# Kernel optimization log

Measured on AMD Instinct MI355X. Metric: run time of the kernel, lower is better.

The kernel has to match this reference:

```python
import jax, jax.numpy as jnp
import numpy as np

EMBED_DIM = 1024
HEADS = 16
HEAD_DIM = EMBED_DIM // HEADS
BATCH = 4
SEQ = 1024


def setup_inputs() -> dict:
    key = jax.random.key(0)
    ks = jax.random.split(key, 9)
    s = 1.0 / np.sqrt(HEAD_DIM)
    so = 1.0 / np.sqrt(EMBED_DIM)
    return {
        "values": jax.random.normal(ks[0], (BATCH, SEQ, EMBED_DIM), dtype=jnp.float32),
        "query": jax.random.normal(ks[1], (BATCH, SEQ, EMBED_DIM), dtype=jnp.float32),
        "key": jax.random.normal(ks[2], (BATCH, SEQ, EMBED_DIM), dtype=jnp.float32),
        "mask": jax.random.randint(ks[3], (BATCH, 1, SEQ, SEQ), 0, 2, dtype=jnp.int32),
        "Wv": jax.random.uniform(ks[4], (HEAD_DIM, HEAD_DIM), jnp.float32, -s, s),
        "Wk": jax.random.uniform(ks[5], (HEAD_DIM, HEAD_DIM), jnp.float32, -s, s),
        "Wq": jax.random.uniform(ks[6], (HEAD_DIM, HEAD_DIM), jnp.float32, -s, s),
        "Wo": jax.random.uniform(ks[7], (EMBED_DIM, EMBED_DIM), jnp.float32, -so, so),
        "bo": jax.random.uniform(ks[8], (EMBED_DIM,), jnp.float32, -so, so),
    }


def reference(values, query, key, mask, Wv, Wk, Wq, Wo, bo):
    N, Lq, E = query.shape
    Lk = key.shape[1]
    H, D = HEADS, HEAD_DIM
    # reshape to heads, then per-head shared linear projection (Linear(head_dim, head_dim), no bias)
    v = jnp.einsum('nlhd,ed->nlhe', values.reshape(N, Lk, H, D), Wv)
    k = jnp.einsum('nlhd,ed->nlhe', key.reshape(N, Lk, H, D), Wk)
    q = jnp.einsum('nlhd,ed->nlhe', query.reshape(N, Lq, H, D), Wq)
    # full [N,H,Q,K] scores, scaled by 1/sqrt(embed_dim) as in source
    sim = jnp.einsum('nqhd,nkhd->nhqk', q, k)
    sim = jnp.where(mask == 0, jnp.float32(-1e20), sim)
    attn = jax.nn.softmax(sim / jnp.sqrt(jnp.float32(E)), axis=3)
    out = jnp.einsum('nhqk,nkhd->nqhd', attn, v).reshape(N, Lq, H * D)
    return out @ Wo.T + bo
```

## Files before the change

kernel.cpp:

```cpp
#include <hip/hip_runtime.h>

#define SEQ 1024
#define HEADS 16
#define HD 64
#define EMB 1024

typedef short bf16x8 __attribute__((ext_vector_type(8)));
typedef float f32x4 __attribute__((ext_vector_type(4)));

static __device__ __forceinline__ unsigned cvtpk(float a, float b) {
  unsigned r;
  asm("v_cvt_pk_bf16_f32 %0, %1, %2" : "=v"(r) : "v"(a), "v"(b));
  return r;
}

static __device__ __forceinline__ void gload_lds16(const void* g, void* l) {
  __builtin_amdgcn_global_load_lds((const __attribute__((address_space(1))) unsigned int*)g,
                                   (__attribute__((address_space(3))) unsigned int*)l,
                                   16, 0, 0);
}

__global__ __launch_bounds__(256) void k_pp(const int* __restrict__ mask,
                                            const float* __restrict__ Wo,
                                            const float* __restrict__ Wv,
                                            const float* __restrict__ Wq,
                                            const float* __restrict__ Wk,
                                            const float* __restrict__ values,
                                            const float* __restrict__ query,
                                            const float* __restrict__ key,
                                            unsigned long long* __restrict__ mb,
                                            unsigned short* __restrict__ wob,
                                            unsigned short* __restrict__ vb,
                                            unsigned short* __restrict__ qb,
                                            unsigned short* __restrict__ kb) {
  __shared__ unsigned short Wl[64][64];
  const unsigned tid = threadIdx.x;
  const unsigned b = blockIdx.x;

  if (b < 3072) {
    const int lane = tid & 63, c = lane & 15, g = lane >> 4;
    const int wid = b * 4 + (tid >> 6);
    const int t = wid >> 12;
    const int rem = wid & 4095;
    const int n = rem >> 10, h = (rem >> 6) & 15, lb = rem & 63;

    const float* x; unsigned short* out;
// ... 62 lines not shown
    } else {
      unsigned short* op = out + ((size_t)(n * HEADS + h) * SEQ + lb * 16) * HD;
      #pragma unroll
      for (int r = 0; r < 4; ++r) {
        const unsigned w0 = cvtpk(acc[0][r], acc[1][r]);
        const unsigned w1 = cvtpk(acc[2][r], acc[3][r]);
        *(uint2*)(op + (4 * g + r) * HD + 4 * c) = make_uint2(w0, w1);
      }
    }
  } else if (b < 7168) {
    const unsigned lane = tid & 63u;
    const unsigned gwb = (b - 3072) * 16u + (tid >> 6) * 4u;
    #pragma unroll
    for (int it = 0; it < 4; ++it) {
      const unsigned gw = gwb + it;
      const int v = mask[(size_t)gw * 64u + lane];
      const unsigned long long bits = __ballot(v != 0);
      if (lane == 0) {
        const unsigned n = gw >> 14, qrow = (gw >> 4) & 1023u, ktile = gw & 15u;
        mb[((size_t)n * 16 + ktile) * 1024 + qrow] = bits;
      }
    }
  } else {
    const unsigned gid = (b - 7168) * 256u + tid;
    const unsigned e = gid >> 8, rem = gid & 255u;
    const unsigned blk = rem >> 4, cc = rem & 15u;
    const float* src = Wo + (size_t)e * 1024 + blk * 64 + cc;
    const unsigned w0 = cvtpk(src[0], src[16]);
    const unsigned w1 = cvtpk(src[32], src[48]);
    *(uint2*)(wob + (size_t)gid * 4) = make_uint2(w0, w1);
  }
}

__global__ __launch_bounds__(256, 2) void k_attn(const unsigned short* __restrict__ qb,
                                                 const unsigned short* __restrict__ kb,
                                                 const unsigned short* __restrict__ vb,
                                                 const unsigned long long* __restrict__ mb,
                                                 unsigned short* __restrict__ ob) {
  const int tid = threadIdx.x;
  const int w = tid >> 6, lane = tid & 63;
  const int c = lane & 15, g = lane >> 4;
  const int bid = blockIdx.x;
  const int nh = bid & 63, q128 = bid >> 6;
  const int n = nh >> 4, h = nh & 15;
  const int qlo = q128 * 128 + w * 32;

  __shared__ unsigned short Ks[2][2][64][64];
  __shared__ unsigned short Vs[2][2][64][64];

  char* const Kb0 = (char*)&Ks[0][0][0][0];
  char* const Vb0 = (char*)&Vs[0][0][0][0];

  const size_t nhb = (size_t)(n * HEADS + h) * (SEQ * HD);
  const unsigned short* qp = qb + nhb;
  const char* kpB = (const char*)(kb + nhb);
  const char* vpB = (const char*)(vb + nhb);

  const char* kSrc[4]; const char* vSrc[4]; int ldsOff[4];
  #pragma unroll
  for (int i = 0; i < 4; ++i) {
    const int off = i * 4096 + tid * 16;
    const int row = off >> 7;
    const int tile = row >> 6, r64 = row & 63;
    const int slot = (off >> 4) & 7;
    const int krow = ((r64 >> 4) & 1) * 32 + ((r64 >> 5) & 1) * 4 +
                     ((r64 >> 2) & 3) * 8 + (r64 & 3);
    const int sw = (slot ^ (r64 & 7)) << 4;
    kSrc[i] = kpB + (size_t)(tile * 64 + krow) * 128 + sw;
    vSrc[i] = vpB + (size_t)r64 * 2048 + tile * 128 + sw;
    ldsOff[i] = off;
  }

  bf16x8 qa[2][2];
  #pragma unroll
  for (int grp = 0; grp < 2; ++grp)
    #pragma unroll
    for (int ks = 0; ks < 2; ++ks)
      qa[grp][ks] = *(const bf16x8*)(qp + (size_t)(qlo + grp * 16 + c) * HD + ks * 32 + g * 8);

  bf16x8 ones;
  #pragma unroll
  for (int j = 0; j < 8; ++j) ones[j] = (short)0x3F80;

  f32x4 o[2][4] = {};
  f32x4 lacc[2] = {};

#define STAGEKV(dstK, dstV, kp_) do {                                    \
    _Pragma("unroll")                                                    \
    for (int i = 0; i < 4; ++i) {                                        \
      gload_lds16(kSrc[i] + (size_t)(kp_) * 16384, (dstK) + ldsOff[i]);  \
      gload_lds16(vSrc[i] + (kp_) * 256, (dstV) + ldsOff[i]);            \
    }                                                                    \
  } while (0)

  STAGEKV(Kb0, Vb0, 0);

  for (int kp = 0; kp < 8; ++kp) {
    const int cur = kp & 1;
    if (kp < 7) {
      STAGEKV(Kb0 + (cur ^ 1) * 16384, Vb0 + (cur ^ 1) * 16384, kp + 1);
      asm volatile("s_waitcnt vmcnt(8)" ::: "memory");
    } else {
      asm volatile("s_waitcnt vmcnt(0)" ::: "memory");
    }
    asm volatile("s_barrier" ::: "memory");

    #pragma unroll
    for (int t = 0; t < 2; ++t) {
      const int kt = kp * 2 + t;
      char* const Kc = Kb0 + cur * 16384 + t * 8192;
      char* const Vc = Vb0 + cur * 16384 + t * 8192;

      const unsigned long long bits0 = mb[((size_t)(n * 16 + kt)) * 1024 + qlo + c];
      const unsigned long long bits1 = mb[((size_t)(n * 16 + kt)) * 1024 + qlo + 16 + c];

      bf16x8 kf[4][2];
      #pragma unroll
      for (int sub = 0; sub < 4; ++sub) {
        const int rho = sub * 16 + c;
        #pragma unroll
        for (int ks = 0; ks < 2; ++ks)
          kf[sub][ks] = *(const bf16x8*)(Kc + rho * 128 + (((ks * 4 + g) ^ (c & 7)) << 4));
      }
      bf16x8 vf[4][2];
      #pragma unroll
      for (int db = 0; db < 4; ++db) {
        const int row = db * 16 + c;
        #pragma unroll
        for (int ks = 0; ks < 2; ++ks)
          vf[db][ks] = *(const bf16x8*)(Vc + row * 128 + (((ks * 4 + g) ^ (c & 7)) << 4));
      }

      #pragma unroll
      for (int grp = 0; grp < 2; ++grp) {
        const unsigned long long bits = grp ? bits1 : bits0;
        const unsigned blo = (unsigned)bits, bhi = (unsigned)(bits >> 32);

        f32x4 s[4];
        __builtin_amdgcn_s_setprio(1);
        #pragma unroll
        for (int sub = 0; sub < 4; ++sub) {
          f32x4 acc = {};
          acc = __builtin_amdgcn_mfma_f32_16x16x32_bf16(kf[sub][0], qa[grp][0], acc, 0, 0, 0);
          acc = __builtin_amdgcn_mfma_f32_16x16x32_bf16(kf[sub][1], qa[grp][1], acc, 0, 0, 0);
          s[sub] = acc;
        }
        __builtin_amdgcn_s_setprio(0);

        unsigned pw[2][4];
        #pragma unroll
        for (int sub = 0; sub < 4; ++sub) {
          const unsigned x = ((sub & 1) ? bhi : blo) >> (8 * g + ((sub >> 1) << 2));
          const float p0 = (x & 1u) ? __builtin_exp2f(s[sub][0]) : 0.f;
          const float p1 = (x & 2u) ? __builtin_exp2f(s[sub][1]) : 0.f;
          const float p2 = (x & 4u) ? __builtin_exp2f(s[sub][2]) : 0.f;
          const float p3 = (x & 8u) ? __builtin_exp2f(s[sub][3]) : 0.f;
          pw[sub & 1][(sub >> 1) * 2 + 0] = cvtpk(p0, p1);
          pw[sub & 1][(sub >> 1) * 2 + 1] = cvtpk(p2, p3);
        }
        bf16x8 pa[2];
        pa[0] = __builtin_bit_cast(bf16x8, *(uint4*)&pw[0][0]);
        pa[1] = __builtin_bit_cast(bf16x8, *(uint4*)&pw[1][0]);

        __builtin_amdgcn_s_setprio(1);
        #pragma unroll
        for (int ks = 0; ks < 2; ++ks) {
          #pragma unroll
          for (int db = 0; db < 4; ++db)
            o[grp][db] = __builtin_amdgcn_mfma_f32_16x16x32_bf16(pa[ks], vf[db][ks], o[grp][db], 0, 0, 0);
          lacc[grp] = __builtin_amdgcn_mfma_f32_16x16x32_bf16(pa[ks], ones, lacc[grp], 0, 0, 0);
        }
        __builtin_amdgcn_s_setprio(0);
      }
    }

    if (kp < 7) asm volatile("s_barrier" ::: "memory");
  }
#undef STAGEKV

  #pragma unroll
  for (int grp = 0; grp < 2; ++grp)
    #pragma unroll
    for (int r = 0; r < 4; ++r) {
      const float inv = 1.0f / lacc[grp][r];
      const unsigned w0 = cvtpk(o[grp][0][r] * inv, o[grp][1][r] * inv);
      const unsigned w1 = cvtpk(o[grp][2][r] * inv, o[grp][3][r] * inv);
      *(uint2*)(ob + ((size_t)n * SEQ + qlo + grp * 16 + 4 * g + r) * EMB + h * 64 + 4 * c) =
          make_uint2(w0, w1);
    }
}

__global__ __launch_bounds__(256, 2) void k_gemm(const unsigned short* __restrict__ A,
                                                 const unsigned short* __restrict__ B,
                                                 const float* __restrict__ bo,
                                                 float* __restrict__ C) {
  const int tid = threadIdx.x;
  const int w = tid >> 6, lane = tid & 63;
  const int c = lane & 15, g = lane >> 4;
  const int bm = blockIdx.x & 31, bn = blockIdx.x >> 5;
  const int m0 = bm * 128, n0 = bn * 64;

  __shared__ unsigned short As[2][128][64];
  __shared__ unsigned short Bs[2][64][64];

  const char* aSrc[4]; int aOff[4];
  const char* bSrc[2]; int bOff[2];
  #pragma unroll
  for (int i = 0; i < 4; ++i) {
    const int off = i * 4096 + tid * 16;
    const int row = off >> 7, slot = (off >> 4) & 7;
    const int sw = (slot ^ (row & 7)) << 4;
    aSrc[i] = (const char*)A + (size_t)(m0 + row) * 2048 + sw;
    aOff[i] = off;
  }
  #pragma unroll
  for (int i = 0; i < 2; ++i) {
    const int off = i * 4096 + tid * 16;
    const int row = off >> 7, slot = (off >> 4) & 7;
    const int sw = (slot ^ (row & 7)) << 4;
    bSrc[i] = (const char*)B + (size_t)(n0 + row) * 2048 + sw;
    bOff[i] = off;
  }
// ... 51 lines not shown

  #pragma unroll
  for (int j = 0; j < 4; ++j) {
    const int col = n0 + j * 16 + c;
    const float bv = bo[col];
    #pragma unroll
    for (int i = 0; i < 2; ++i) {
      const int rowb = m0 + w * 32 + i * 16 + 4 * g;
      #pragma unroll
      for (int r = 0; r < 4; ++r)
        C[(size_t)(rowb + r) * 1024 + col] = acc[i][j][r] + bv;
    }
  }
}

extern "C" void kernel_launch(void* const* d_in, const int* in_sizes, int n_in,
                              void* d_out, int out_size, void* d_ws, size_t ws_size,
                              hipStream_t stream) {
  const float* values = (const float*)d_in[0];
  const float* query  = (const float*)d_in[1];
  const float* key    = (const float*)d_in[2];
  const int*   mask   = (const int*)d_in[3];
  const float* Wv     = (const float*)d_in[4];
  const float* Wk     = (const float*)d_in[5];
  const float* Wq     = (const float*)d_in[6];
  const float* Wo     = (const float*)d_in[7];
  const float* bo     = (const float*)d_in[8];
  float* out = (float*)d_out;

  char* ws = (char*)d_ws;
  unsigned short* qb = (unsigned short*)(ws);
  unsigned short* kb = (unsigned short*)(ws + (size_t)8 * 1024 * 1024);
  unsigned short* vb = (unsigned short*)(ws + (size_t)16 * 1024 * 1024);
  unsigned short* ob = (unsigned short*)(ws + (size_t)24 * 1024 * 1024);
  unsigned long long* mb = (unsigned long long*)(ws + (size_t)32 * 1024 * 1024);
  unsigned short* wob = (unsigned short*)(ws + (size_t)33 * 1024 * 1024);

  k_pp<<<8192, 256, 0, stream>>>(mask, Wo, Wv, Wq, Wk, values, query, key, mb, wob, vb, qb, kb);
  k_attn<<<512, 256, 0, stream>>>(qb, kb, vb, mb, ob);
  k_gemm<<<512, 256, 0, stream>>>(ob, wob, bo, out);
}
```

Before: 76.77 us.

## Split attention over two key halves with a separate merge kernel

The attention kernel now splits the key dimension in two, launching twice as many blocks with smaller LDS tiles and higher occupancy (launch bounds 4). Each block writes unnormalized partial outputs in bf16 plus row sums, and a new merge kernel adds the halves, normalizes, and writes the head-interleaved output into the reused qb buffer. The mask bits for the block are staged into LDS up front instead of being read from global memory per tile. This aims to fill more CUs, at the cost of an extra launch, extra partial-result traffic, and an added bf16 rounding of the partial sums.

Measured after the change: 133.7 us. 74.2% more time.

```diff
diff --git a/kernel.cpp b/kernel.cpp
--- a/kernel.cpp
+++ b/kernel.cpp
@@ -12,6 +12,13 @@
   unsigned r;
   asm("v_cvt_pk_bf16_f32 %0, %1, %2" : "=v"(r) : "v"(a), "v"(b));
   return r;
+}
+
+static __device__ __forceinline__ float bflo(unsigned u) {
+  return __builtin_bit_cast(float, u << 16);
+}
+static __device__ __forceinline__ float bfhi(unsigned u) {
+  return __builtin_bit_cast(float, u & 0xffff0000u);
 }
 
 static __device__ __forceinline__ void gload_lds16(const void* g, void* l) {
@@ -140,162 +147,202 @@
   }
 }
 
-__global__ __launch_bounds__(256, 2) void k_attn(const unsigned short* __restrict__ qb,
+__global__ __launch_bounds__(256, 4) void k_attn(const unsigned short* __restrict__ qb,
                                                  const unsigned short* __restrict__ kb,
                                                  const unsigned short* __restrict__ vb,
                                                  const unsigned long long* __restrict__ mb,
-                                                 unsigned short* __restrict__ ob) {
+                                                 unsigned short* __restrict__ opart,
+                                                 float* __restrict__ lpart) {
   const int tid = threadIdx.x;
   const int w = tid >> 6, lane = tid & 63;
   const int c = lane & 15, g = lane >> 4;
   const int bid = blockIdx.x;
+  const int khalf = bid >> 9;
+  const int rem = bid & 511;
+  const int q128 = rem >> 6, nh = rem & 63;
+  const int n = nh >> 4, h = nh & 15;
+  const int qlo = q128 * 128 + w * 32;
+  const int kt0 = khalf * 8;
+
+  __shared__ unsigned short Ks[2][64][64];
+  __shared__ unsigned short Vs[2][64][64];
+  __shared__ unsigned long long Ml[8][128];
+
+  char* const Kb0 = (char*)&Ks[0][0][0];
+  char* const Vb0 = (char*)&Vs[0][0][0];
+  char* const Mb0 = (char*)&Ml[0][0];
+
+  const size_t nhb = (size_t)(n * HEADS + h) * (SEQ * HD);
+  const unsigned short* qp = qb + nhb;
+  const char* kpB = (const char*)(kb + nhb) + (size_t)kt0 * 8192;
+  const char* vpB = (const char*)(vb + nhb) + kt0 * 128;
+
+  const char* kSrc[2]; const char* vSrc[2]; int ldsOff[2];
+  #pragma unroll
+  for (int i = 0; i < 2; ++i) {
+    const int off = i * 4096 + tid * 16;
+    const int row = off >> 7, slot = (off >> 4) & 7;
+    const int krow = ((row >> 4) & 1) * 32 + ((row >> 5) & 1) * 4 +
+                     ((row >> 2) & 3) * 8 + (row & 3);
+    const int sw = (slot ^ (row & 7)) << 4;
+    kSrc[i] = kpB + krow * 128 + sw;
+    vSrc[i] = vpB + (size_t)row * 2048 + sw;
+    ldsOff[i] = off;
+  }
+
+  bf16x8 qa[2][2];
+  #pragma unroll
+  for (int grp = 0; grp < 2; ++grp)
+    #pragma unroll
+    for (int ks = 0; ks < 2; ++ks)
+      qa[grp][ks] = *(const bf16x8*)(qp + (size_t)(qlo + grp * 16 + c) * HD + ks * 32 + g * 8);
+
+  bf16x8 ones;
+  #pragma unroll
+  for (int j = 0; j < 8; ++j) ones[j] = (short)0x3F80;
+
+  f32x4 o[2][4] = {};
+  f32x4 lacc[2] = {};
+
+#define STAGEKV(dstK, dstV, kt_) do {                                   \
+    _Pragma("unroll")                                                   \
+    for (int i = 0; i < 2; ++i) {                                       \
+      gload_lds16(kSrc[i] + (size_t)(kt_) * 8192, (dstK) + ldsOff[i]);  \
+      gload_lds16(vSrc[i] + (kt_) * 128, (dstV) + ldsOff[i]);           \
+    }                                                                   \
+  } while (0)
+
+  #pragma unroll
+  for (int i = 0; i < 2; ++i) {
+    const int moff = i * 4096 + tid * 16;
+    const int mkt = moff >> 10;
+    const char* msrc = (const char*)mb +
+        ((size_t)(n * 16 + kt0 + mkt) * 1024 + q128 * 128) * 8 + (moff & 1023);
+    gload_lds16(msrc, Mb0 + moff);
+  }
+  STAGEKV(Kb0, Vb0, 0);
+
+  for (int kt = 0; kt < 8; ++kt) {
+    const int cur = kt & 1;
+    char* const Kc = Kb0 + cur * 8192;
+    char* const Vc = Vb0 + cur * 8192;
+    if (kt < 7) {
+      STAGEKV(Kb0 + (cur ^ 1) * 8192, Vb0 + (cur ^ 1) * 8192, kt + 1);
+      asm volatile("s_waitcnt vmcnt(4)" ::: "memory");
+    } else {
+      asm volatile("s_waitcnt vmcnt(0)" ::: "memory");
+    }
+    asm volatile("s_barrier" ::: "memory");
+
+    const unsigned long long bits0 = Ml[kt][w * 32 + c];
+    const unsigned long long bits1 = Ml[kt][w * 32 + 16 + c];
+
+    bf16x8 kf[4][2];
+    #pragma unroll
+    for (int sub = 0; sub < 4; ++sub) {
+      const int rho = sub * 16 + c;
+      #pragma unroll
+      for (int ks = 0; ks < 2; ++ks)
+        kf[sub][ks] = *(const bf16x8*)(Kc + rho * 128 + (((ks * 4 + g) ^ (c & 7)) << 4));
+    }
+    bf16x8 vf[4][2];
+    #pragma unroll
+    for (int db = 0; db < 4; ++db) {
+      const int row = db * 16 + c;
+      #pragma unroll
+      for (int ks = 0; ks < 2; ++ks)
+        vf[db][ks] = *(const bf16x8*)(Vc + row * 128 + (((ks * 4 + g) ^ (c & 7)) << 4));
+    }
+
+    #pragma unroll
+    for (int grp = 0; grp < 2; ++grp) {
+      const unsigned long long bits = grp ? bits1 : bits0;
+      const unsigned blo = (unsigned)bits, bhi = (unsigned)(bits >> 32);
+
+      f32x4 s[4];
+      __builtin_amdgcn_s_setprio(1);
+      #pragma unroll
+      for (int sub = 0; sub < 4; ++sub) {
+        f32x4 acc = {};
+        acc = __builtin_amdgcn_mfma_f32_16x16x32_bf16(kf[sub][0], qa[grp][0], acc, 0, 0, 0);
+        acc = __builtin_amdgcn_mfma_f32_16x16x32_bf16(kf[sub][1], qa[grp][1], acc, 0, 0, 0);
+        s[sub] = acc;
+      }
+      __builtin_amdgcn_s_setprio(0);
+
+      unsigned pw[2][4];
+      #pragma unroll
+      for (int sub = 0; sub < 4; ++sub) {
+        const unsigned x = ((sub & 1) ? bhi : blo) >> (8 * g + ((sub >> 1) << 2));
+        const float p0 = (x & 1u) ? __builtin_exp2f(s[sub][0]) : 0.f;
+        const float p1 = (x & 2u) ? __builtin_exp2f(s[sub][1]) : 0.f;
+        const float p2 = (x & 4u) ? __builtin_exp2f(s[sub][2]) : 0.f;
+        const float p3 = (x & 8u) ? __builtin_exp2f(s[sub][3]) : 0.f;
+        pw[sub & 1][(sub >> 1) * 2 + 0] = cvtpk(p0, p1);
+        pw[sub & 1][(sub >> 1) * 2 + 1] = cvtpk(p2, p3);
+      }
+      bf16x8 pa[2];
+      pa[0] = __builtin_bit_cast(bf16x8, *(uint4*)&pw[0][0]);
+      pa[1] = __builtin_bit_cast(bf16x8, *(uint4*)&pw[1][0]);
+
+      __builtin_amdgcn_s_setprio(1);
+      #pragma unroll
+      for (int ks = 0; ks < 2; ++ks) {
+        #pragma unroll
+        for (int db = 0; db < 4; ++db)
+          o[grp][db] = __builtin_amdgcn_mfma_f32_16x16x32_bf16(pa[ks], vf[db][ks], o[grp][db], 0, 0, 0);
+        lacc[grp] = __builtin_amdgcn_mfma_f32_16x16x32_bf16(pa[ks], ones, lacc[grp], 0, 0, 0);
+      }
+      __builtin_amdgcn_s_setprio(0);
+    }
+
+    if (kt < 7) asm volatile("s_barrier" ::: "memory");
+  }
+#undef STAGEKV
+
+  unsigned short* opb = opart + ((size_t)(khalf * 64 + nh) * 1024) * 64;
+  float* lpb = lpart + (size_t)(khalf * 64 + nh) * 1024;
+  #pragma unroll
+  for (int grp = 0; grp < 2; ++grp)
+    #pragma unroll
+    for (int r = 0; r < 4; ++r) {
+      const int qrow = qlo + grp * 16 + 4 * g + r;
+      const unsigned w0 = cvtpk(o[grp][0][r], o[grp][1][r]);
+      const unsigned w1 = cvtpk(o[grp][2][r], o[grp][3][r]);
+      *(uint2*)(opb + (size_t)qrow * 64 + 4 * c) = make_uint2(w0, w1);
+      if (c == 0) lpb[qrow] = lacc[grp][r];
+    }
+}
+
+__global__ __launch_bounds__(256) void k_merge(const unsigned short* __restrict__ opart,
+                                               const float* __restrict__ lpart,
+                                               unsigned short* __restrict__ om) {
+  const int bid = blockIdx.x;
   const int nh = bid & 63, q128 = bid >> 6;
   const int n = nh >> 4, h = nh & 15;
-  const int qlo = q128 * 128 + w * 32;
-
-  __shared__ unsigned short Ks[2][2][64][64];
-  __shared__ unsigned short Vs[2][2][64][64];
-
-  char* const Kb0 = (char*)&Ks[0][0][0][0];
-  char* const Vb0 = (char*)&Vs[0][0][0][0];
-
-  const size_t nhb = (size_t)(n * HEADS + h) * (SEQ * HD);
-  const unsigned short* qp = qb + nhb;
-  const char* kpB = (const char*)(kb + nhb);
-  const char* vpB = (const char*)(vb + nhb);
-
-  const char* kSrc[4]; const char* vSrc[4]; int ldsOff[4];
-  #pragma unroll
-  for (int i = 0; i < 4; ++i) {
-    const int off = i * 4096 + tid * 16;
-    const int row = off >> 7;
-    const int tile = row >> 6, r64 = row & 63;
-    const int slot = (off >> 4) & 7;
-    const int krow = ((r64 >> 4) & 1) * 32 + ((r64 >> 5) & 1) * 4 +
-                     ((r64 >> 2) & 3) * 8 + (r64 & 3);
-    const int sw = (slot ^ (r64 & 7)) << 4;
-    kSrc[i] = kpB + (size_t)(tile * 64 + krow) * 128 + sw;
-    vSrc[i] = vpB + (size_t)r64 * 2048 + tile * 128 + sw;
-    ldsOff[i] = off;
-  }
-
-  bf16x8 qa[2][2];
-  #pragma unroll
-  for (int grp = 0; grp < 2; ++grp)
-    #pragma unroll
-    for (int ks = 0; ks < 2; ++ks)
-      qa[grp][ks] = *(const bf16x8*)(qp + (size_t)(qlo + grp * 16 + c) * HD + ks * 32 + g * 8);
-
-  bf16x8 ones;
-  #pragma unroll
-  for (int j = 0; j < 8; ++j) ones[j] = (short)0x3F80;
-
-  f32x4 o[2][4] = {};
-  f32x4 lacc[2] = {};
-
-#define STAGEKV(dstK, dstV, kp_) do {                                    \
-    _Pragma("unroll")                                                    \
-    for (int i = 0; i < 4; ++i) {                                        \
-      gload_lds16(kSrc[i] + (size_t)(kp_) * 16384, (dstK) + ldsOff[i]);  \
-      gload_lds16(vSrc[i] + (kp_) * 256, (dstV) + ldsOff[i]);            \
-    }                                                                    \
-  } while (0)
-
-  STAGEKV(Kb0, Vb0, 0);
-
-  for (int kp = 0; kp < 8; ++kp) {
-    const int cur = kp & 1;
-    if (kp < 7) {
-      STAGEKV(Kb0 + (cur ^ 1) * 16384, Vb0 + (cur ^ 1) * 16384, kp + 1);
-      asm volatile("s_waitcnt vmcnt(8)" ::: "memory");
-    } else {
-      asm volatile("s_waitcnt vmcnt(0)" ::: "memory");
-    }
-    asm volatile("s_barrier" ::: "memory");
-
-    #pragma unroll
-    for (int t = 0; t < 2; ++t) {
-      const int kt = kp * 2 + t;
-      char* const Kc = Kb0 + cur * 16384 + t * 8192;
-      char* const Vc = Vb0 + cur * 16384 + t * 8192;
-
-      const unsigned long long bits0 = mb[((size_t)(n * 16 + kt)) * 1024 + qlo + c];
-      const unsigned long long bits1 = mb[((size_t)(n * 16 + kt)) * 1024 + qlo + 16 + c];
-
-      bf16x8 kf[4][2];
-      #pragma unroll
-      for (int sub = 0; sub < 4; ++sub) {
-        const int rho = sub * 16 + c;
-        #pragma unroll
-        for (int ks = 0; ks < 2; ++ks)
-          kf[sub][ks] = *(const bf16x8*)(Kc + rho * 128 + (((ks * 4 + g) ^ (c & 7)) << 4));
-      }
-      bf16x8 vf[4][2];
-      #pragma unroll
-      for (int db = 0; db < 4; ++db) {
-        const int row = db * 16 + c;
-        #pragma unroll
-        for (int ks = 0; ks < 2; ++ks)
-          vf[db][ks] = *(const bf16x8*)(Vc + row * 128 + (((ks * 4 + g) ^ (c & 7)) << 4));
-      }
-
-      #pragma unroll
-      for (int grp = 0; grp < 2; ++grp) {
-        const unsigned long long bits = grp ? bits1 : bits0;
-        const unsigned blo = (unsigned)bits, bhi = (unsigned)(bits >> 32);
-
-        f32x4 s[4];
-        __builtin_amdgcn_s_setprio(1);
-        #pragma unroll
-        for (int sub = 0; sub < 4; ++sub) {
-          f32x4 acc = {};
-          acc = __builtin_amdgcn_mfma_f32_16x16x32_bf16(kf[sub][0], qa[grp][0], acc, 0, 0, 0);
-          acc = __builtin_amdgcn_mfma_f32_16x16x32_bf16(kf[sub][1], qa[grp][1], acc, 0, 0, 0);
-          s[sub] = acc;
-        }
-        __builtin_amdgcn_s_setprio(0);
-
-        unsigned pw[2][4];
-        #pragma unroll
-        for (int sub = 0; sub < 4; ++sub) {
-          const unsigned x = ((sub & 1) ? bhi : blo) >> (8 * g + ((sub >> 1) << 2));
-          const float p0 = (x & 1u) ? __builtin_exp2f(s[sub][0]) : 0.f;
-          const float p1 = (x & 2u) ? __builtin_exp2f(s[sub][1]) : 0.f;
-          const float p2 = (x & 4u) ? __builtin_exp2f(s[sub][2]) : 0.f;
-          const float p3 = (x & 8u) ? __builtin_exp2f(s[sub][3]) : 0.f;
-          pw[sub & 1][(sub >> 1) * 2 + 0] = cvtpk(p0, p1);
-          pw[sub & 1][(sub >> 1) * 2 + 1] = cvtpk(p2, p3);
-        }
-        bf16x8 pa[2];
-        pa[0] = __builtin_bit_cast(bf16x8, *(uint4*)&pw[0][0]);
-        pa[1] = __builtin_bit_cast(bf16x8, *(uint4*)&pw[1][0]);
-
-        __builtin_amdgcn_s_setprio(1);
-        #pragma unroll
-        for (int ks = 0; ks < 2; ++ks) {
-          #pragma unroll
-          for (int db = 0; db < 4; ++db)
-            o[grp][db] = __builtin_amdgcn_mfma_f32_16x16x32_bf16(pa[ks], vf[db][ks], o[grp][db], 0, 0, 0);
-          lacc[grp] = __builtin_amdgcn_mfma_f32_16x16x32_bf16(pa[ks], ones, lacc[grp], 0, 0, 0);
-        }
-        __builtin_amdgcn_s_setprio(0);
-      }
-    }
-
-    if (kp < 7) asm volatile("s_barrier" ::: "memory");
-  }
-#undef STAGEKV
-
-  #pragma unroll
-  for (int grp = 0; grp < 2; ++grp)
-    #pragma unroll
-    for (int r = 0; r < 4; ++r) {
-      const float inv = 1.0f / lacc[grp][r];
-      const unsigned w0 = cvtpk(o[grp][0][r] * inv, o[grp][1][r] * inv);
-      const unsigned w1 = cvtpk(o[grp][2][r] * inv, o[grp][3][r] * inv);
-      *(uint2*)(ob + ((size_t)n * SEQ + qlo + grp * 16 + 4 * g + r) * EMB + h * 64 + 4 * c) =
-          make_uint2(w0, w1);
-    }
+  const int tid = threadIdx.x;
+
+  #pragma unroll
+  for (int it = 0; it < 4; ++it) {
+    const int idx = it * 256 + tid;
+    const int qrow = q128 * 128 + (idx >> 3);
+    const int dc = (idx & 7) * 8;
+    const size_t off = ((size_t)nh * 1024 + qrow) * 64 + dc;
+    const uint4 a = *(const uint4*)(opart + off);
+    const uint4 b2 = *(const uint4*)(opart + (size_t)4194304 + off);
+    const float l = lpart[nh * 1024 + qrow] + lpart[65536 + nh * 1024 + qrow];
+    const float inv = 1.0f / l;
+    const unsigned* au = (const unsigned*)&a;
+    const unsigned* bu = (const unsigned*)&b2;
+    unsigned ow[4];
+    #pragma unroll
+    for (int j = 0; j < 4; ++j) {
+      const float s0 = bflo(au[j]) + bflo(bu[j]);
+      const float s1 = bfhi(au[j]) + bfhi(bu[j]);
+      ow[j] = cvtpk(s0 * inv, s1 * inv);
+    }
+    *(uint4*)(om + ((size_t)(n * 1024 + qrow)) * 1024 + h * 64 + dc) = *(uint4*)ow;
+  }
 }
 
 __global__ __launch_bounds__(256, 2) void k_gemm(const unsigned short* __restrict__ A,
@@ -413,11 +460,13 @@
   unsigned short* qb = (unsigned short*)(ws);
   unsigned short* kb = (unsigned short*)(ws + (size_t)8 * 1024 * 1024);
   unsigned short* vb = (unsigned short*)(ws + (size_t)16 * 1024 * 1024);
-  unsigned short* ob = (unsigned short*)(ws + (size_t)24 * 1024 * 1024);
-  unsigned long long* mb = (unsigned long long*)(ws + (size_t)32 * 1024 * 1024);
-  unsigned short* wob = (unsigned short*)(ws + (size_t)33 * 1024 * 1024);
+  unsigned short* opart = (unsigned short*)(ws + (size_t)24 * 1024 * 1024);
+  unsigned long long* mb = (unsigned long long*)(ws + (size_t)40 * 1024 * 1024);
+  float* lpart = (float*)(ws + (size_t)40 * 1024 * 1024 + 512 * 1024);
+  unsigned short* wob = (unsigned short*)(ws + (size_t)41 * 1024 * 1024);
 
   k_pp<<<8192, 256, 0, stream>>>(mask, Wo, Wv, Wq, Wk, values, query, key, mb, wob, vb, qb, kb);
-  k_attn<<<512, 256, 0, stream>>>(qb, kb, vb, mb, ob);
-  k_gemm<<<512, 256, 0, stream>>>(ob, wob, bo, out);
-}
+  k_attn<<<1024, 256, 0, stream>>>(qb, kb, vb, mb, opart, lpart);
+  k_merge<<<512, 256, 0, stream>>>(opart, lpart, qb);
+  k_gemm<<<512, 256, 0, stream>>>(qb, wob, bo, out);
+}
```

## Halve attention query tile, stage mask bits in LDS, raise occupancy

Applied to the files above, without the earlier changes.

The attention kernel now handles 64 query rows per block (16 per wave) instead of 128, doubling the grid to 1024 blocks and raising launch bounds to four blocks per CU. K/V staging drops from two 64-key tiles per step to one, which halves LDS use, and the mask bitfields for the block are preloaded once into LDS instead of read from global memory each step. This targets better occupancy and latency hiding. The cost is that each K/V tile is now reused by half as many query rows, so total K/V traffic doubles and there are twice as many barriers per key.

Measured after the change: 77.56 us. Within noise of the previous version (+1.0%).

```diff
diff --git a/kernel.cpp b/kernel.cpp
--- a/kernel.cpp
+++ b/kernel.cpp
@@ -140,7 +140,7 @@
   }
 }
 
-__global__ __launch_bounds__(256, 2) void k_attn(const unsigned short* __restrict__ qb,
+__global__ __launch_bounds__(256, 4) void k_attn(const unsigned short* __restrict__ qb,
                                                  const unsigned short* __restrict__ kb,
                                                  const unsigned short* __restrict__ vb,
                                                  const unsigned long long* __restrict__ mb,
@@ -149,153 +149,147 @@
   const int w = tid >> 6, lane = tid & 63;
   const int c = lane & 15, g = lane >> 4;
   const int bid = blockIdx.x;
-  const int nh = bid & 63, q128 = bid >> 6;
+  const int nh = bid & 63, q64 = bid >> 6;
   const int n = nh >> 4, h = nh & 15;
-  const int qlo = q128 * 128 + w * 32;
-
-  __shared__ unsigned short Ks[2][2][64][64];
-  __shared__ unsigned short Vs[2][2][64][64];
-
-  char* const Kb0 = (char*)&Ks[0][0][0][0];
-  char* const Vb0 = (char*)&Vs[0][0][0][0];
+  const int qlo = q64 * 64 + w * 16;
+
+  __shared__ unsigned short Ks[2][64][64];
+  __shared__ unsigned short Vs[2][64][64];
+  __shared__ unsigned long long Ml[16][64];
+
+  char* const Kb0 = (char*)&Ks[0][0][0];
+  char* const Vb0 = (char*)&Vs[0][0][0];
+  char* const Mb0 = (char*)&Ml[0][0];
 
   const size_t nhb = (size_t)(n * HEADS + h) * (SEQ * HD);
   const unsigned short* qp = qb + nhb;
   const char* kpB = (const char*)(kb + nhb);
   const char* vpB = (const char*)(vb + nhb);
 
-  const char* kSrc[4]; const char* vSrc[4]; int ldsOff[4];
-  #pragma unroll
-  for (int i = 0; i < 4; ++i) {
+  const char* kSrc[2]; const char* vSrc[2]; int ldsOff[2];
+  #pragma unroll
+  for (int i = 0; i < 2; ++i) {
     const int off = i * 4096 + tid * 16;
-    const int row = off >> 7;
-    const int tile = row >> 6, r64 = row & 63;
-    const int slot = (off >> 4) & 7;
-    const int krow = ((r64 >> 4) & 1) * 32 + ((r64 >> 5) & 1) * 4 +
-                     ((r64 >> 2) & 3) * 8 + (r64 & 3);
-    const int sw = (slot ^ (r64 & 7)) << 4;
-    kSrc[i] = kpB + (size_t)(tile * 64 + krow) * 128 + sw;
-    vSrc[i] = vpB + (size_t)r64 * 2048 + tile * 128 + sw;
+    const int row = off >> 7, slot = (off >> 4) & 7;
+    const int krow = ((row >> 4) & 1) * 32 + ((row >> 5) & 1) * 4 +
+                     ((row >> 2) & 3) * 8 + (row & 3);
+    const int sw = (slot ^ (row & 7)) << 4;
+    kSrc[i] = kpB + krow * 128 + sw;
+    vSrc[i] = vpB + (size_t)row * 2048 + sw;
     ldsOff[i] = off;
   }
 
-  bf16x8 qa[2][2];
-  #pragma unroll
-  for (int grp = 0; grp < 2; ++grp)
-    #pragma unroll
-    for (int ks = 0; ks < 2; ++ks)
-      qa[grp][ks] = *(const bf16x8*)(qp + (size_t)(qlo + grp * 16 + c) * HD + ks * 32 + g * 8);
+  bf16x8 qa[2];
+  #pragma unroll
+  for (int ks = 0; ks < 2; ++ks)
+    qa[ks] = *(const bf16x8*)(qp + (size_t)(qlo + c) * HD + ks * 32 + g * 8);
 
   bf16x8 ones;
   #pragma unroll
   for (int j = 0; j < 8; ++j) ones[j] = (short)0x3F80;
 
-  f32x4 o[2][4] = {};
-  f32x4 lacc[2] = {};
-
-#define STAGEKV(dstK, dstV, kp_) do {                                    \
-    _Pragma("unroll")                                                    \
-    for (int i = 0; i < 4; ++i) {                                        \
-      gload_lds16(kSrc[i] + (size_t)(kp_) * 16384, (dstK) + ldsOff[i]);  \
-      gload_lds16(vSrc[i] + (kp_) * 256, (dstV) + ldsOff[i]);            \
-    }                                                                    \
+  f32x4 o[4] = {};
+  f32x4 lacc = {};
+
+#define STAGEKV(dstK, dstV, kt_) do {                                   \
+    _Pragma("unroll")                                                   \
+    for (int i = 0; i < 2; ++i) {                                       \
+      gload_lds16(kSrc[i] + (size_t)(kt_) * 8192, (dstK) + ldsOff[i]);  \
+      gload_lds16(vSrc[i] + (kt_) * 128, (dstV) + ldsOff[i]);           \
+    }                                                                   \
   } while (0)
 
+  #pragma unroll
+  for (int i = 0; i < 2; ++i) {
+    const int moff = i * 4096 + tid * 16;
+    const int mkt = moff >> 9;
+    const char* msrc = (const char*)mb +
+        ((size_t)(n * 16 + mkt) * 1024 + q64 * 64) * 8 + (moff & 511);
+    gload_lds16(msrc, Mb0 + moff);
+  }
   STAGEKV(Kb0, Vb0, 0);
 
-  for (int kp = 0; kp < 8; ++kp) {
-    const int cur = kp & 1;
-    if (kp < 7) {
-      STAGEKV(Kb0 + (cur ^ 1) * 16384, Vb0 + (cur ^ 1) * 16384, kp + 1);
-      asm volatile("s_waitcnt vmcnt(8)" ::: "memory");
+  for (int kt = 0; kt < 16; ++kt) {
+    const int cur = kt & 1;
+    char* const Kc = Kb0 + cur * 8192;
+    char* const Vc = Vb0 + cur * 8192;
+    if (kt < 15) {
+      STAGEKV(Kb0 + (cur ^ 1) * 8192, Vb0 + (cur ^ 1) * 8192, kt + 1);
+      asm volatile("s_waitcnt vmcnt(4)" ::: "memory");
     } else {
       asm volatile("s_waitcnt vmcnt(0)" ::: "memory");
     }
     asm volatile("s_barrier" ::: "memory");
 
-    #pragma unroll
-    for (int t = 0; t < 2; ++t) {
-      const int kt = kp * 2 + t;
-      char* const Kc = Kb0 + cur * 16384 + t * 8192;
-      char* const Vc = Vb0 + cur * 16384 + t * 8192;
-
-      const unsigned long long bits0 = mb[((size_t)(n * 16 + kt)) * 1024 + qlo + c];
-      const unsigned long long bits1 = mb[((size_t)(n * 16 + kt)) * 1024 + qlo + 16 + c];
-
-      bf16x8 kf[4][2];
-      #pragma unroll
-      for (int sub = 0; sub < 4; ++sub) {
-        const int rho = sub * 16 + c;
-        #pragma unroll
-        for (int ks = 0; ks < 2; ++ks)
-          kf[sub][ks] = *(const bf16x8*)(Kc + rho * 128 + (((ks * 4 + g) ^ (c & 7)) << 4));
-      }
-      bf16x8 vf[4][2];
-      #pragma unroll
-      for (int db = 0; db < 4; ++db) {
-        const int row = db * 16 + c;
-        #pragma unroll
-        for (int ks = 0; ks < 2; ++ks)
-          vf[db][ks] = *(const bf16x8*)(Vc + row * 128 + (((ks * 4 + g) ^ (c & 7)) << 4));
-      }
-
-      #pragma unroll
-      for (int grp = 0; grp < 2; ++grp) {
-        const unsigned long long bits = grp ? bits1 : bits0;
-        const unsigned blo = (unsigned)bits, bhi = (unsigned)(bits >> 32);
-
-        f32x4 s[4];
-        __builtin_amdgcn_s_setprio(1);
-        #pragma unroll
-        for (int sub = 0; sub < 4; ++sub) {
-          f32x4 acc = {};
-          acc = __builtin_amdgcn_mfma_f32_16x16x32_bf16(kf[sub][0], qa[grp][0], acc, 0, 0, 0);
-          acc = __builtin_amdgcn_mfma_f32_16x16x32_bf16(kf[sub][1], qa[grp][1], acc, 0, 0, 0);
-          s[sub] = acc;
-        }
-        __builtin_amdgcn_s_setprio(0);
-
-        unsigned pw[2][4];
-        #pragma unroll
-        for (int sub = 0; sub < 4; ++sub) {
-          const unsigned x = ((sub & 1) ? bhi : blo) >> (8 * g + ((sub >> 1) << 2));
-          const float p0 = (x & 1u) ? __builtin_exp2f(s[sub][0]) : 0.f;
-          const float p1 = (x & 2u) ? __builtin_exp2f(s[sub][1]) : 0.f;
-          const float p2 = (x & 4u) ? __builtin_exp2f(s[sub][2]) : 0.f;
-          const float p3 = (x & 8u) ? __builtin_exp2f(s[sub][3]) : 0.f;
-          pw[sub & 1][(sub >> 1) * 2 + 0] = cvtpk(p0, p1);
-          pw[sub & 1][(sub >> 1) * 2 + 1] = cvtpk(p2, p3);
-        }
-        bf16x8 pa[2];
-        pa[0] = __builtin_bit_cast(bf16x8, *(uint4*)&pw[0][0]);
-        pa[1] = __builtin_bit_cast(bf16x8, *(uint4*)&pw[1][0]);
-
-        __builtin_amdgcn_s_setprio(1);
-        #pragma unroll
-        for (int ks = 0; ks < 2; ++ks) {
-          #pragma unroll
-          for (int db = 0; db < 4; ++db)
-            o[grp][db] = __builtin_amdgcn_mfma_f32_16x16x32_bf16(pa[ks], vf[db][ks], o[grp][db], 0, 0, 0);
-          lacc[grp] = __builtin_amdgcn_mfma_f32_16x16x32_bf16(pa[ks], ones, lacc[grp], 0, 0, 0);
-        }
-        __builtin_amdgcn_s_setprio(0);
-      }
-    }
-
-    if (kp < 7) asm volatile("s_barrier" ::: "memory");
+    const unsigned long long bits = Ml[kt][w * 16 + c];
+    const unsigned blo = (unsigned)bits, bhi = (unsigned)(bits >> 32);
+
+    bf16x8 kf[4][2];
+    #pragma unroll
+    for (int sub = 0; sub < 4; ++sub) {
+      const int rho = sub * 16 + c;
+      #pragma unroll
+      for (int ks = 0; ks < 2; ++ks)
+        kf[sub][ks] = *(const bf16x8*)(Kc + rho * 128 + (((ks * 4 + g) ^ (c & 7)) << 4));
+    }
+
+    f32x4 s[4];
+    __builtin_amdgcn_s_setprio(1);
+    #pragma unroll
+    for (int sub = 0; sub < 4; ++sub) {
+      f32x4 acc = {};
+      acc = __builtin_amdgcn_mfma_f32_16x16x32_bf16(kf[sub][0], qa[0], acc, 0, 0, 0);
+      acc = __builtin_amdgcn_mfma_f32_16x16x32_bf16(kf[sub][1], qa[1], acc, 0, 0, 0);
+      s[sub] = acc;
+    }
+    __builtin_amdgcn_s_setprio(0);
+
+    bf16x8 vf[4][2];
+    #pragma unroll
+    for (int db = 0; db < 4; ++db) {
+      const int row = db * 16 + c;
+      #pragma unroll
+      for (int ks = 0; ks < 2; ++ks)
+        vf[db][ks] = *(const bf16x8*)(Vc + row * 128 + (((ks * 4 + g) ^ (c & 7)) << 4));
+    }
+
+    unsigned pw[2][4];
+    #pragma unroll
+    for (int sub = 0; sub < 4; ++sub) {
+      const unsigned x = ((sub & 1) ? bhi : blo) >> (8 * g + ((sub >> 1) << 2));
+      const float p0 = (x & 1u) ? __builtin_exp2f(s[sub][0]) : 0.f;
+      const float p1 = (x & 2u) ? __builtin_exp2f(s[sub][1]) : 0.f;
+      const float p2 = (x & 4u) ? __builtin_exp2f(s[sub][2]) : 0.f;
+      const float p3 = (x & 8u) ? __builtin_exp2f(s[sub][3]) : 0.f;
+      pw[sub & 1][(sub >> 1) * 2 + 0] = cvtpk(p0, p1);
+      pw[sub & 1][(sub >> 1) * 2 + 1] = cvtpk(p2, p3);
+    }
+    bf16x8 pa[2];
+    pa[0] = __builtin_bit_cast(bf16x8, *(uint4*)&pw[0][0]);
+    pa[1] = __builtin_bit_cast(bf16x8, *(uint4*)&pw[1][0]);
+
+    __builtin_amdgcn_s_setprio(1);
+    #pragma unroll
+    for (int ks = 0; ks < 2; ++ks) {
+      #pragma unroll
+      for (int db = 0; db < 4; ++db)
+        o[db] = __builtin_amdgcn_mfma_f32_16x16x32_bf16(pa[ks], vf[db][ks], o[db], 0, 0, 0);
+      lacc = __builtin_amdgcn_mfma_f32_16x16x32_bf16(pa[ks], ones, lacc, 0, 0, 0);
+    }
+    __builtin_amdgcn_s_setprio(0);
+
+    if (kt < 15) asm volatile("s_barrier" ::: "memory");
   }
 #undef STAGEKV
 
   #pragma unroll
-  for (int grp = 0; grp < 2; ++grp)
-    #pragma unroll
-    for (int r = 0; r < 4; ++r) {
-      const float inv = 1.0f / lacc[grp][r];
-      const unsigned w0 = cvtpk(o[grp][0][r] * inv, o[grp][1][r] * inv);
-      const unsigned w1 = cvtpk(o[grp][2][r] * inv, o[grp][3][r] * inv);
-      *(uint2*)(ob + ((size_t)n * SEQ + qlo + grp * 16 + 4 * g + r) * EMB + h * 64 + 4 * c) =
-          make_uint2(w0, w1);
-    }
+  for (int r = 0; r < 4; ++r) {
+    const float inv = 1.0f / lacc[r];
+    const unsigned w0 = cvtpk(o[0][r] * inv, o[1][r] * inv);
+    const unsigned w1 = cvtpk(o[2][r] * inv, o[3][r] * inv);
+    *(uint2*)(ob + ((size_t)n * SEQ + qlo + 4 * g + r) * EMB + h * 64 + 4 * c) =
+        make_uint2(w0, w1);
+  }
 }
 
 __global__ __launch_bounds__(256, 2) void k_gemm(const unsigned short* __restrict__ A,
@@ -418,6 +412,6 @@
   unsigned short* wob = (unsigned short*)(ws + (size_t)33 * 1024 * 1024);
 
   k_pp<<<8192, 256, 0, stream>>>(mask, Wo, Wv, Wq, Wk, values, query, key, mb, wob, vb, qb, kb);
-  k_attn<<<512, 256, 0, stream>>>(qb, kb, vb, mb, ob);
+  k_attn<<<1024, 256, 0, stream>>>(qb, kb, vb, mb, ob);
   k_gemm<<<512, 256, 0, stream>>>(ob, wob, bo, out);
 }
```

## Split attention along keys across waves with LDS partial-sum reduction

Applied to the files above, without the earlier changes.

The attention kernel now gives each block 64 queries instead of 128 and doubles the grid. Inside a block, the four waves each handle a quarter of the key range over the same queries, each staging K/V into its own LDS slot without block barriers. Partial outputs and row sums are then reduced through LDS. The goal is more parallelism and no per-tile block synchronisation. In exchange it adds a reduction step, stores the partial outputs as bf16 (losing some precision), and uses 64KB of LDS per block, which may limit occupancy.

Measured after the change: 81.43 us. +6.1%, slower.

```diff
diff --git a/kernel.cpp b/kernel.cpp
--- a/kernel.cpp
+++ b/kernel.cpp
@@ -12,6 +12,13 @@
   unsigned r;
   asm("v_cvt_pk_bf16_f32 %0, %1, %2" : "=v"(r) : "v"(a), "v"(b));
   return r;
+}
+
+static __device__ __forceinline__ float bflo(unsigned u) {
+  return __builtin_bit_cast(float, u << 16);
+}
+static __device__ __forceinline__ float bfhi(unsigned u) {
+  return __builtin_bit_cast(float, u & 0xffff0000u);
 }
 
 static __device__ __forceinline__ void gload_lds16(const void* g, void* l) {
@@ -149,153 +156,186 @@
   const int w = tid >> 6, lane = tid & 63;
   const int c = lane & 15, g = lane >> 4;
   const int bid = blockIdx.x;
-  const int nh = bid & 63, q128 = bid >> 6;
+  const int nh = bid & 63, q64 = bid >> 6;
   const int n = nh >> 4, h = nh & 15;
-  const int qlo = q128 * 128 + w * 32;
-
-  __shared__ unsigned short Ks[2][2][64][64];
-  __shared__ unsigned short Vs[2][2][64][64];
-
-  char* const Kb0 = (char*)&Ks[0][0][0][0];
-  char* const Vb0 = (char*)&Vs[0][0][0][0];
+  const int qlo = q64 * 64;
+
+  __shared__ char LDSA[65536];
+  char* const slot = LDSA + w * 16384;
 
   const size_t nhb = (size_t)(n * HEADS + h) * (SEQ * HD);
   const unsigned short* qp = qb + nhb;
-  const char* kpB = (const char*)(kb + nhb);
-  const char* vpB = (const char*)(vb + nhb);
-
-  const char* kSrc[4]; const char* vSrc[4]; int ldsOff[4];
-  #pragma unroll
-  for (int i = 0; i < 4; ++i) {
-    const int off = i * 4096 + tid * 16;
-    const int row = off >> 7;
-    const int tile = row >> 6, r64 = row & 63;
-    const int slot = (off >> 4) & 7;
-    const int krow = ((r64 >> 4) & 1) * 32 + ((r64 >> 5) & 1) * 4 +
-                     ((r64 >> 2) & 3) * 8 + (r64 & 3);
-    const int sw = (slot ^ (r64 & 7)) << 4;
-    kSrc[i] = kpB + (size_t)(tile * 64 + krow) * 128 + sw;
-    vSrc[i] = vpB + (size_t)r64 * 2048 + tile * 128 + sw;
-    ldsOff[i] = off;
-  }
-
-  bf16x8 qa[2][2];
-  #pragma unroll
-  for (int grp = 0; grp < 2; ++grp)
+  const char* kpB = (const char*)(kb + nhb) + (size_t)(w * 256) * 128;
+  const char* vpB = (const char*)(vb + nhb) + (size_t)(w * 256) * 2;
+
+  bf16x8 qa[4][2];
+  #pragma unroll
+  for (int grp = 0; grp < 4; ++grp)
     #pragma unroll
     for (int ks = 0; ks < 2; ++ks)
       qa[grp][ks] = *(const bf16x8*)(qp + (size_t)(qlo + grp * 16 + c) * HD + ks * 32 + g * 8);
 
+  const char* kS[4]; const char* vS[4]; int sO[4];
+  #pragma unroll
+  for (int i = 0; i < 4; ++i) {
+    const int off = i * 1024 + lane * 16;
+    sO[i] = off;
+    const int rho = off >> 7, sl = (off >> 4) & 7;
+    const int kap = 4 * (rho >> 4) + 8 * ((rho >> 2) & 3) + (rho & 3);
+    kS[i] = kpB + (size_t)kap * 128 + ((sl ^ (rho & 7)) << 4);
+    const int d = off >> 6, sl2 = (off >> 4) & 3;
+    vS[i] = vpB + (size_t)d * 2048 + ((sl2 ^ ((d >> 1) & 3)) << 4);
+  }
+
+  const char* const mgb = (const char*)mb + ((size_t)(n * 16) * 1024 + qlo + c) * 8;
+
   bf16x8 ones;
   #pragma unroll
   for (int j = 0; j < 8; ++j) ones[j] = (short)0x3F80;
 
-  f32x4 o[2][4] = {};
-  f32x4 lacc[2] = {};
-
-#define STAGEKV(dstK, dstV, kp_) do {                                    \
-    _Pragma("unroll")                                                    \
-    for (int i = 0; i < 4; ++i) {                                        \
-      gload_lds16(kSrc[i] + (size_t)(kp_) * 16384, (dstK) + ldsOff[i]);  \
-      gload_lds16(vSrc[i] + (kp_) * 256, (dstV) + ldsOff[i]);            \
-    }                                                                    \
+  f32x4 o[4][4] = {};
+  f32x4 lac[4] = {};
+  unsigned mcur[4], mnxt[4];
+
+#define STG(buf, t_) do {                                               \
+    char* const db_ = slot + (buf) * 8192;                              \
+    _Pragma("unroll")                                                   \
+    for (int i = 0; i < 4; ++i) {                                       \
+      gload_lds16(kS[i] + (size_t)(t_) * 4096, db_ + sO[i]);            \
+      gload_lds16(vS[i] + (t_) * 64, db_ + 4096 + sO[i]);               \
+    }                                                                   \
   } while (0)
 
-  STAGEKV(Kb0, Vb0, 0);
-
-  for (int kp = 0; kp < 8; ++kp) {
-    const int cur = kp & 1;
-    if (kp < 7) {
-      STAGEKV(Kb0 + (cur ^ 1) * 16384, Vb0 + (cur ^ 1) * 16384, kp + 1);
-      asm volatile("s_waitcnt vmcnt(8)" ::: "memory");
+  #pragma unroll
+  for (int grp = 0; grp < 4; ++grp)
+    mnxt[grp] = *(const unsigned*)(mgb + grp * 128 + (size_t)(w * 4) * 8192);
+  STG(0, 0);
+
+  for (int t = 0; t < 8; ++t) {
+    const int cur = t & 1;
+    #pragma unroll
+    for (int grp = 0; grp < 4; ++grp) mcur[grp] = mnxt[grp];
+
+    if (t < 7) {
+      const int ktg1 = w * 8 + t + 1;
+      #pragma unroll
+      for (int grp = 0; grp < 4; ++grp)
+        mnxt[grp] = *(const unsigned*)(mgb + grp * 128 +
+                                       (size_t)(ktg1 >> 1) * 8192 + (ktg1 & 1) * 4);
+      STG(cur ^ 1, t + 1);
+      asm volatile("s_waitcnt vmcnt(12)" ::: "memory");
     } else {
       asm volatile("s_waitcnt vmcnt(0)" ::: "memory");
     }
-    asm volatile("s_barrier" ::: "memory");
-
-    #pragma unroll
-    for (int t = 0; t < 2; ++t) {
-      const int kt = kp * 2 + t;
-      char* const Kc = Kb0 + cur * 16384 + t * 8192;
-      char* const Vc = Vb0 + cur * 16384 + t * 8192;
-
-      const unsigned long long bits0 = mb[((size_t)(n * 16 + kt)) * 1024 + qlo + c];
-      const unsigned long long bits1 = mb[((size_t)(n * 16 + kt)) * 1024 + qlo + 16 + c];
-
-      bf16x8 kf[4][2];
-      #pragma unroll
-      for (int sub = 0; sub < 4; ++sub) {
-        const int rho = sub * 16 + c;
-        #pragma unroll
-        for (int ks = 0; ks < 2; ++ks)
-          kf[sub][ks] = *(const bf16x8*)(Kc + rho * 128 + (((ks * 4 + g) ^ (c & 7)) << 4));
-      }
-      bf16x8 vf[4][2];
+    char* const Kc = slot + cur * 8192;
+    char* const Vc = Kc + 4096;
+
+    bf16x8 kf[2][2];
+    #pragma unroll
+    for (int sub = 0; sub < 2; ++sub) {
+      const int rho = sub * 16 + c;
+      #pragma unroll
+      for (int ks = 0; ks < 2; ++ks)
+        kf[sub][ks] = *(const bf16x8*)(Kc + rho * 128 + (((ks * 4 + g) ^ (c & 7)) << 4));
+    }
+    bf16x8 vf[4];
+    #pragma unroll
+    for (int db = 0; db < 4; ++db) {
+      const int d = db * 16 + c;
+      vf[db] = *(const bf16x8*)(Vc + d * 64 + ((g ^ ((c >> 1) & 3)) << 4));
+    }
+
+    #pragma unroll
+    for (int grp = 0; grp < 4; ++grp) {
+      f32x4 s0 = {}, s1 = {};
+      __builtin_amdgcn_s_setprio(1);
+      s0 = __builtin_amdgcn_mfma_f32_16x16x32_bf16(kf[0][0], qa[grp][0], s0, 0, 0, 0);
+      s0 = __builtin_amdgcn_mfma_f32_16x16x32_bf16(kf[0][1], qa[grp][1], s0, 0, 0, 0);
+      s1 = __builtin_amdgcn_mfma_f32_16x16x32_bf16(kf[1][0], qa[grp][0], s1, 0, 0, 0);
+      s1 = __builtin_amdgcn_mfma_f32_16x16x32_bf16(kf[1][1], qa[grp][1], s1, 0, 0, 0);
+      __builtin_amdgcn_s_setprio(0);
+
+      const unsigned x = mcur[grp] >> (8 * g);
+      const float p0 = (x & 1u)   ? __builtin_exp2f(s0[0]) : 0.f;
+      const float p1 = (x & 2u)   ? __builtin_exp2f(s0[1]) : 0.f;
+      const float p2 = (x & 4u)   ? __builtin_exp2f(s0[2]) : 0.f;
+      const float p3 = (x & 8u)   ? __builtin_exp2f(s0[3]) : 0.f;
+      const float p4 = (x & 16u)  ? __builtin_exp2f(s1[0]) : 0.f;
+      const float p5 = (x & 32u)  ? __builtin_exp2f(s1[1]) : 0.f;
+      const float p6 = (x & 64u)  ? __builtin_exp2f(s1[2]) : 0.f;
+      const float p7 = (x & 128u) ? __builtin_exp2f(s1[3]) : 0.f;
+      const uint4 pu = make_uint4(cvtpk(p0, p1), cvtpk(p2, p3),
+                                  cvtpk(p4, p5), cvtpk(p6, p7));
+      const bf16x8 pa = __builtin_bit_cast(bf16x8, pu);
+
+      __builtin_amdgcn_s_setprio(1);
+      #pragma unroll
+      for (int db = 0; db < 4; ++db)
+        o[grp][db] = __builtin_amdgcn_mfma_f32_16x16x32_bf16(pa, vf[db], o[grp][db], 0, 0, 0);
+      lac[grp] = __builtin_amdgcn_mfma_f32_16x16x32_bf16(pa, ones, lac[grp], 0, 0, 0);
+      __builtin_amdgcn_s_setprio(0);
+    }
+  }
+#undef STG
+
+  auto storeO = [&](int x) {
+    char* const obw = LDSA + x * 8192;
+    #pragma unroll
+    for (int grp = 0; grp < 4; ++grp) {
+      const int slt = grp * 2 + (g >> 1);
       #pragma unroll
       for (int db = 0; db < 4; ++db) {
-        const int row = db * 16 + c;
-        #pragma unroll
-        for (int ks = 0; ks < 2; ++ks)
-          vf[db][ks] = *(const bf16x8*)(Vc + row * 128 + (((ks * 4 + g) ^ (c & 7)) << 4));
-      }
-
-      #pragma unroll
-      for (int grp = 0; grp < 2; ++grp) {
-        const unsigned long long bits = grp ? bits1 : bits0;
-        const unsigned blo = (unsigned)bits, bhi = (unsigned)(bits >> 32);
-
-        f32x4 s[4];
-        __builtin_amdgcn_s_setprio(1);
-        #pragma unroll
-        for (int sub = 0; sub < 4; ++sub) {
-          f32x4 acc = {};
-          acc = __builtin_amdgcn_mfma_f32_16x16x32_bf16(kf[sub][0], qa[grp][0], acc, 0, 0, 0);
-          acc = __builtin_amdgcn_mfma_f32_16x16x32_bf16(kf[sub][1], qa[grp][1], acc, 0, 0, 0);
-          s[sub] = acc;
-        }
-        __builtin_amdgcn_s_setprio(0);
-
-        unsigned pw[2][4];
-        #pragma unroll
-        for (int sub = 0; sub < 4; ++sub) {
-          const unsigned x = ((sub & 1) ? bhi : blo) >> (8 * g + ((sub >> 1) << 2));
-          const float p0 = (x & 1u) ? __builtin_exp2f(s[sub][0]) : 0.f;
-          const float p1 = (x & 2u) ? __builtin_exp2f(s[sub][1]) : 0.f;
-          const float p2 = (x & 4u) ? __builtin_exp2f(s[sub][2]) : 0.f;
-          const float p3 = (x & 8u) ? __builtin_exp2f(s[sub][3]) : 0.f;
-          pw[sub & 1][(sub >> 1) * 2 + 0] = cvtpk(p0, p1);
-          pw[sub & 1][(sub >> 1) * 2 + 1] = cvtpk(p2, p3);
-        }
-        bf16x8 pa[2];
-        pa[0] = __builtin_bit_cast(bf16x8, *(uint4*)&pw[0][0]);
-        pa[1] = __builtin_bit_cast(bf16x8, *(uint4*)&pw[1][0]);
-
-        __builtin_amdgcn_s_setprio(1);
-        #pragma unroll
-        for (int ks = 0; ks < 2; ++ks) {
-          #pragma unroll
-          for (int db = 0; db < 4; ++db)
-            o[grp][db] = __builtin_amdgcn_mfma_f32_16x16x32_bf16(pa[ks], vf[db][ks], o[grp][db], 0, 0, 0);
-          lacc[grp] = __builtin_amdgcn_mfma_f32_16x16x32_bf16(pa[ks], ones, lacc[grp], 0, 0, 0);
-        }
-        __builtin_amdgcn_s_setprio(0);
-      }
-    }
-
-    if (kp < 7) asm volatile("s_barrier" ::: "memory");
-  }
-#undef STAGEKV
-
-  #pragma unroll
-  for (int grp = 0; grp < 2; ++grp)
-    #pragma unroll
-    for (int r = 0; r < 4; ++r) {
-      const float inv = 1.0f / lacc[grp][r];
-      const unsigned w0 = cvtpk(o[grp][0][r] * inv, o[grp][1][r] * inv);
-      const unsigned w1 = cvtpk(o[grp][2][r] * inv, o[grp][3][r] * inv);
-      *(uint2*)(ob + ((size_t)n * SEQ + qlo + grp * 16 + 4 * g + r) * EMB + h * 64 + 4 * c) =
-          make_uint2(w0, w1);
-    }
+        const int d = db * 16 + c;
+        *(uint2*)(obw + d * 128 + ((slt ^ (d & 7)) << 4) + 8 * (g & 1)) =
+            make_uint2(cvtpk(o[grp][db][0], o[grp][db][1]),
+                       cvtpk(o[grp][db][2], o[grp][db][3]));
+      }
+    }
+    if (c == 0) {
+      float* const lw = (float*)(LDSA + 32768 + x * 256);
+      #pragma unroll
+      for (int grp = 0; grp < 4; ++grp)
+        *(f32x4*)(lw + grp * 16 + 4 * g) = lac[grp];
+    }
+  };
+  auto loadO = [&](int x) {
+    const char* const obr = LDSA + x * 8192;
+    #pragma unroll
+    for (int grp = 0; grp < 4; ++grp) {
+      const int slt = grp * 2 + (g >> 1);
+      #pragma unroll
+      for (int db = 0; db < 4; ++db) {
+        const int d = db * 16 + c;
+        const uint2 u = *(const uint2*)(obr + d * 128 + ((slt ^ (d & 7)) << 4) + 8 * (g & 1));
+        o[grp][db][0] += bflo(u.x); o[grp][db][1] += bfhi(u.x);
+        o[grp][db][2] += bflo(u.y); o[grp][db][3] += bfhi(u.y);
+      }
+    }
+    const float* const lr = (const float*)(LDSA + 32768 + x * 256);
+    #pragma unroll
+    for (int grp = 0; grp < 4; ++grp)
+      lac[grp] += *(const f32x4*)(lr + grp * 16 + 4 * g);
+  };
+
+  __syncthreads();
+  if (w & 1) storeO(w);
+  __syncthreads();
+  if (w == 0) loadO(1);
+  if (w == 2) { loadO(3); storeO(2); }
+  __syncthreads();
+  if (w == 0) {
+    loadO(2);
+    #pragma unroll
+    for (int grp = 0; grp < 4; ++grp)
+      #pragma unroll
+      for (int r = 0; r < 4; ++r) {
+        const float inv = 1.0f / lac[grp][r];
+        const unsigned w0 = cvtpk(o[grp][0][r] * inv, o[grp][1][r] * inv);
+        const unsigned w1 = cvtpk(o[grp][2][r] * inv, o[grp][3][r] * inv);
+        *(uint2*)(ob + ((size_t)n * SEQ + qlo + grp * 16 + 4 * g + r) * EMB +
+                  h * 64 + 4 * c) = make_uint2(w0, w1);
+      }
+  }
 }
 
 __global__ __launch_bounds__(256, 2) void k_gemm(const unsigned short* __restrict__ A,
@@ -418,6 +458,6 @@
   unsigned short* wob = (unsigned short*)(ws + (size_t)33 * 1024 * 1024);
 
   k_pp<<<8192, 256, 0, stream>>>(mask, Wo, Wv, Wq, Wk, values, query, key, mb, wob, vb, qb, kb);
-  k_attn<<<512, 256, 0, stream>>>(qb, kb, vb, mb, ob);
+  k_attn<<<1024, 256, 0, stream>>>(qb, kb, vb, mb, ob);
   k_gemm<<<512, 256, 0, stream>>>(ob, wob, bo, out);
 }
```
